# Kernel tuning notes

Measured on AMD Instinct MI355X. Metric: run time of the kernel, lower is better.

Reference implementation:

```python
import jax, jax.numpy as jnp
import numpy as np

B, FEW, D = 128, 64, 512
E, O, H, K = 16, 512, 64, 3


def setup_inputs() -> dict:
    key = jax.random.key(0)
    ks = jax.random.split(key, 9)
    s_d = 1.0 / np.sqrt(D)
    s_h = 1.0 / np.sqrt(H)
    x = jax.random.normal(ks[0], (B, FEW, D), dtype=jnp.float32)
    # gating network params (Linear(D,64), Linear(64,E))
    gW1 = jax.random.uniform(ks[1], (D, H), jnp.float32, -s_d, s_d)
    gb1 = jax.random.uniform(ks[2], (H,), jnp.float32, -s_d, s_d)
    gW2 = jax.random.uniform(ks[3], (H, E), jnp.float32, -s_h, s_h)
    gb2 = jax.random.uniform(ks[4], (E,), jnp.float32, -s_h, s_h)
    # stacked expert params: fc1 Linear(D,64), fc2 Linear(64,O) per expert
    W1 = jax.random.uniform(ks[5], (E, D, H), jnp.float32, -s_d, s_d)
    b1 = jax.random.uniform(ks[6], (E, H), jnp.float32, -s_d, s_d)
    W2 = jax.random.uniform(ks[7], (E, H, O), jnp.float32, -s_h, s_h)
    b2 = jax.random.uniform(ks[8], (E, O), jnp.float32, -s_h, s_h)
    return {"x": x, "gW1": gW1, "gb1": gb1, "gW2": gW2, "gb2": gb2,
            "W1": W1, "b1": b1, "W2": W2, "b2": b2}


def reference(x, gW1, gb1, gW2, gb2, W1, b1, W2, b2):
    b, few, d = x.shape
    t = x.reshape(b * few, d)                                   # [T, D]
    # gating: relu(Linear) -> Linear -> softmax over experts
    gates = jax.nn.softmax(jax.nn.relu(t @ gW1 + gb1) @ gW2 + gb2, axis=-1)
    gates = gates.reshape(b, few, -1)                           # [B, few, E]
    # dense all-expert compute (matches torch stack over ModuleList)
    h = jax.nn.relu(jnp.einsum('td,edh->teh', t, W1) + b1)      # [T, E, H]
    eo = jnp.einsum('teh,eho->teo', h, W2) + b2                 # [T, E, O]
    eo = eo.reshape(b, few, eo.shape[1], -1)                    # [B, few, E, O]
    # top-k gate values and gather corresponding expert outputs
    topv, topi = jax.lax.top_k(gates, K)                        # [B, few, K]
    sel = jnp.take_along_axis(eo, topi[..., None], axis=2)      # [B, few, K, O]
    out = jnp.sum(sel * topv[..., None], axis=2)                # [B, few, O]
    out = jnp.mean(out, axis=1, keepdims=True)                  # [B, 1, O]
    return out[:, :, None, :]                                   # [B, 1, 1, O]
```

## Files before the change

kernel.cpp:

```cpp
#include <hip/hip_runtime.h>
#include <math.h>

constexpr int Bn  = 128;
constexpr int FEW = 64;
constexpr int Dd  = 512;
constexpr int En  = 16;
constexpr int On  = 512;
constexpr int Hn  = 64;
constexpr int Tn  = Bn * FEW;


__global__ __launch_bounds__(256) void k_gate(
    const float* __restrict__ x, const float* __restrict__ gW1,
    const float* __restrict__ gb1, const float* __restrict__ gW2,
    const float* __restrict__ gb2, int* __restrict__ topi,
    float* __restrict__ topv)
{
    __shared__ float g1l[16 * 65];
    __shared__ float logl[16 * 17];
    __shared__ float w2l[64 * 16];
    __shared__ float b2l[16];

    const int tid = threadIdx.x;
    const int ln  = tid & 63;
    const int wv  = tid >> 6;
    const int t0  = blockIdx.x * 16;
    const int tw  = __builtin_amdgcn_readfirstlane(t0 + wv * 4);

    #pragma unroll
    for (int k = 0; k < 4; k++) w2l[tid + k * 256] = gW2[tid + k * 256];
    if (tid < 16) b2l[tid] = gb2[tid];

    float acc[4];
    const float gb1v = gb1[ln];
    #pragma unroll
    for (int i = 0; i < 4; i++) acc[i] = gb1v;

    const float* xt0 = x + (size_t)tw * Dd;

    float  wc[8];
    float4 xa[4], xb[4];
    #pragma unroll
    for (int j = 0; j < 8; j++) wc[j] = gW1[j * 64 + ln];
    #pragma unroll
    for (int i = 0; i < 4; i++) {
        xa[i] = *(const float4*)(xt0 + i * Dd);
        xb[i] = *(const float4*)(xt0 + i * Dd + 4);
    }

    for (int d = 0; d < 512; d += 8) {
        const int dn = (d + 8) & 511;
        float  wn[8];
        float4 xc[4], xd[4];
        #pragma unroll
        for (int j = 0; j < 8; j++) wn[j] = gW1[(dn + j) * 64 + ln];
        #pragma unroll
        for (int i = 0; i < 4; i++) {
            xc[i] = *(const float4*)(xt0 + i * Dd + dn);
            xd[i] = *(const float4*)(xt0 + i * Dd + dn + 4);
        }
        #pragma unroll
        for (int j = 0; j < 4; j++)
            #pragma unroll
            for (int i = 0; i < 4; i++)
                acc[i] = fmaf(((const float*)&xa[i])[j], wc[j], acc[i]);
        #pragma unroll
        for (int j = 0; j < 4; j++)
            #pragma unroll
            for (int i = 0; i < 4; i++)
                acc[i] = fmaf(((const float*)&xb[i])[j], wc[j + 4], acc[i]);
        #pragma unroll
        for (int j = 0; j < 8; j++) wc[j] = wn[j];
        #pragma unroll
        for (int i = 0; i < 4; i++) { xa[i] = xc[i]; xb[i] = xd[i]; }
    }

    #pragma unroll
    for (int i = 0; i < 4; i++) g1l[(wv * 4 + i) * 65 + ln] = fmaxf(acc[i], 0.f);
    __syncthreads();

    {
        const int tok = tid >> 4;
        const int e   = tid & 15;
        float s = b2l[e];
        const float* g = &g1l[tok * 65];
        #pragma unroll 8
        for (int h = 0; h < 64; h++) s = fmaf(g[h], w2l[h * 16 + e], s);
        logl[tok * 17 + e] = s;
    }
    __syncthreads();

    if (tid < 16) {
        float v[16];
        float mx = -1e30f;
        #pragma unroll
        for (int e = 0; e < 16; e++) { v[e] = logl[tid * 17 + e]; mx = fmaxf(mx, v[e]); }
        float ssum = 0.f;
        #pragma unroll
        for (int e = 0; e < 16; e++) { v[e] = __expf(v[e] - mx); ssum += v[e]; }
        const float inv = 1.f / ssum;
        #pragma unroll
        for (int e = 0; e < 16; e++) v[e] *= inv;
        const int t = t0 + tid;
        unsigned mask = 0;
        for (int j = 0; j < 3; j++) {
            float bv = -1.f; int bi = 0;
            for (int e = 0; e < 16; e++) {
                if (!(mask & (1u << e)) && v[e] > bv) { bv = v[e]; bi = e; }
            }
            mask |= (1u << bi);
            topi[t * 4 + j] = bi;
            topv[t * 4 + j] = bv;
        }
    }
}

__global__ __launch_bounds__(256) void k_expert(
    const float* __restrict__ x, const float* __restrict__ W1,
    const float* __restrict__ b1, const int* __restrict__ topi,
    const float* __restrict__ topv, float* __restrict__ A,
    float* __restrict__ gsum)
{
    __shared__ int   lt[128];
    __shared__ float lv[128];
    __shared__ float Ap[2 * 64];
    __shared__ float gp[2];
    __shared__ int   cnt;

    const int tid = threadIdx.x;
    const int ln  = tid & 63;
    const int wv  = tid >> 6;
    const int e   = blockIdx.x >> 6;
    const int s   = blockIdx.x & 63;
    const int ts  = s * 128;

    if (tid == 0) cnt = 0;
    if (tid < 128) Ap[tid] = 0.f;
    if (tid < 2) gp[tid] = 0.f;
    __syncthreads();

    if (tid < 128) {
        const int t = ts + tid;
        const int4   ti = *(const int4*)(topi + t * 4);
        const float4 tv = *(const float4*)(topv + t * 4);
        const int   idx[3] = { ti.x, ti.y, ti.z };
        const float val[3] = { tv.x, tv.y, tv.z };
        #pragma unroll
        for (int j = 0; j < 3; j++) {
            if (idx[j] == e) {
                const int p = atomicAdd(&cnt, 1);
                lt[p] = tid;
                lv[p] = val[j];
                atomicAdd(&gp[tid >> 6], val[j]);
            }
        }
    }
    __syncthreads();
    const int n = cnt;

    const float b1v = b1[e * 64 + ln];
    const float* __restrict__ W1e = W1 + (size_t)e * (Dd * Hn);

    for (int r0 = wv * 8; r0 < n; r0 += 32) {
        const float* xt[8];
        float mvv[8];
        int   bl[8];
        #pragma unroll
        for (int i = 0; i < 8; i++) {
            const int p = r0 + i;
            int   t = (p < n) ? lt[p] : 0;
            float v = (p < n) ? lv[p] : 0.f;
            t = __builtin_amdgcn_readfirstlane(t);
            xt[i]  = x + (size_t)(ts + t) * Dd;
            mvv[i] = v;
            bl[i]  = t >> 6;
        }
        float acc[8];
        #pragma unroll
        for (int i = 0; i < 8; i++) acc[i] = 0.f;

        float  wc[4];
        float4 xc[8];
        #pragma unroll
        for (int j = 0; j < 4; j++) wc[j] = W1e[j * 64 + ln];
        #pragma unroll
        for (int i = 0; i < 8; i++) xc[i] = *(const float4*)(xt[i]);

        for (int d = 0; d < 512; d += 4) {
            const int dn = (d + 4) & 511;
            float  wn[4];
            float4 xn[8];
            #pragma unroll
            for (int j = 0; j < 4; j++) wn[j] = W1e[(dn + j) * 64 + ln];
            #pragma unroll
            for (int i = 0; i < 8; i++) xn[i] = *(const float4*)(xt[i] + dn);
            #pragma unroll
            for (int j = 0; j < 4; j++)
                #pragma unroll
                for (int i = 0; i < 8; i++)
                    acc[i] = fmaf(((const float*)&xc[i])[j], wc[j], acc[i]);
            #pragma unroll
            for (int j = 0; j < 4; j++) wc[j] = wn[j];
            #pragma unroll
            for (int i = 0; i < 8; i++) xc[i] = xn[i];
        }

        #pragma unroll
        for (int i = 0; i < 8; i++) {
            const float h = fmaxf(acc[i] + b1v, 0.f);
            atomicAdd(&Ap[bl[i] * 64 + ln], mvv[i] * h);
        }
    }
    __syncthreads();

    if (tid < 128) {
        const int bl2 = tid >> 6, h = tid & 63;
        A[(size_t)(s * 2 + bl2) * (En * Hn) + e * 64 + h] = Ap[tid];
    }
    if (tid < 2) gsum[(s * 2 + tid) * En + e] = gp[tid];
}

__global__ __launch_bounds__(256) void k_out(
    const float* __restrict__ W2, const float* __restrict__ b2,
    const float* __restrict__ A, const float* __restrict__ gsum,
    float* __restrict__ out)
{
    __shared__ float Al[4096];
    __shared__ float gl[64];

    const int tid = threadIdx.x;
    const int bq  = blockIdx.x >> 3;
    const int oc  = blockIdx.x & 7;
    const int b0  = bq * 4;
    const int bh  = tid >> 6;
    const int o   = oc * 64 + (tid & 63);

    #pragma unroll
    for (int k = 0; k < 4; k++)
        ((float4*)Al)[tid + k * 256] = ((const float4*)(A + (size_t)b0 * 1024))[tid + k * 256];
    if (tid < 64) gl[tid] = gsum[b0 * En + tid];
    __syncthreads();

    const int ab = bh * 1024;
    float a = 0.f;
    const float* w2p = W2 + o;

    float wc[8];
    #pragma unroll
    for (int j = 0; j < 8; j++) wc[j] = w2p[j * On];

    for (int eh = 0; eh < 1024; eh += 8) {
        const int en = (eh + 8) & 1023;
        float wn[8];
        #pragma unroll
        for (int j = 0; j < 8; j++) wn[j] = w2p[(size_t)(en + j) * On];
        #pragma unroll
        for (int j = 0; j < 8; j++) a = fmaf(Al[ab + eh + j], wc[j], a);
        #pragma unroll
        for (int j = 0; j < 8; j++) wc[j] = wn[j];
    }
    #pragma unroll
    for (int ee = 0; ee < 16; ee++) a = fmaf(gl[bh * 16 + ee], b2[ee * On + o], a);

    out[(size_t)(b0 + bh) * On + o] = a * (1.f / 64.f);
}

extern "C" void kernel_launch(void* const* d_in, const int* in_sizes, int n_in,
                              void* d_out, int out_size, void* d_ws, size_t ws_size,
                              hipStream_t stream)
{
    (void)in_sizes; (void)n_in; (void)out_size; (void)ws_size;
    const float* x   = (const float*)d_in[0];
    const float* gW1 = (const float*)d_in[1];
    const float* gb1 = (const float*)d_in[2];
    const float* gW2 = (const float*)d_in[3];
    const float* gb2 = (const float*)d_in[4];
    const float* W1  = (const float*)d_in[5];
    const float* b1  = (const float*)d_in[6];
    const float* W2  = (const float*)d_in[7];
    const float* b2  = (const float*)d_in[8];
    float* out = (float*)d_out;

    char* ws = (char*)d_ws;
    int*   topi = (int*)(ws);
    float* topv = (float*)(ws + 131072);
    float* A    = (float*)(ws + 262144);
    float* gsum = (float*)(ws + 786432);

    k_gate  <<<dim3(512),  dim3(256), 0, stream>>>(x, gW1, gb1, gW2, gb2, topi, topv);
    k_expert<<<dim3(1024), dim3(256), 0, stream>>>(x, W1, b1, topi, topv, A, gsum);
    k_out   <<<dim3(256),  dim3(256), 0, stream>>>(W2, b2, A, gsum, out);
}
```

Before: 245.5 us.

## Stage token activations and expert weights in LDS for gate and expert kernels

The gate kernel now loads its 16 tokens' activations into shared memory and reads them from LDS, where before each wave read them straight from global memory. The expert kernel tiles W1 into 128-row LDS chunks shared by all four waves, and stages the gathered token rows into LDS, so each weight element is fetched from global memory once per block rather than once per wave. The output kernel switches to vectorized float4 LDS reads. The cost is extra __syncthreads barriers and a much larger LDS footprint (about 48KB in the expert kernel), which can lower occupancy, and there is no double buffering to hide the load latency.

```diff
diff --git a/kernel.cpp b/kernel.cpp
--- a/kernel.cpp
+++ b/kernel.cpp
@@ -1,13 +1,10 @@
 #include <hip/hip_runtime.h>
 #include <math.h>
 
-constexpr int Bn  = 128;
-constexpr int FEW = 64;
 constexpr int Dd  = 512;
 constexpr int En  = 16;
 constexpr int On  = 512;
 constexpr int Hn  = 64;
-constexpr int Tn  = Bn * FEW;
 
 
 __global__ __launch_bounds__(256) void k_gate(
@@ -16,6 +13,7 @@
     const float* __restrict__ gb2, int* __restrict__ topi,
     float* __restrict__ topv)
 {
+    __shared__ float xlds[16 * 512];
     __shared__ float g1l[16 * 65];
     __shared__ float logl[16 * 17];
     __shared__ float w2l[64 * 16];
@@ -25,54 +23,45 @@
     const int ln  = tid & 63;
     const int wv  = tid >> 6;
     const int t0  = blockIdx.x * 16;
-    const int tw  = __builtin_amdgcn_readfirstlane(t0 + wv * 4);
 
     #pragma unroll
     for (int k = 0; k < 4; k++) w2l[tid + k * 256] = gW2[tid + k * 256];
     if (tid < 16) b2l[tid] = gb2[tid];
 
+    #pragma unroll
+    for (int k = 0; k < 8; k++) {
+        const int f   = tid + k * 256;
+        const int tok = f >> 7;
+        const int df4 = f & 127;
+        ((float4*)xlds)[f] =
+            *(const float4*)(x + (size_t)(t0 + tok) * Dd + df4 * 4);
+    }
+    __syncthreads();
+
     float acc[4];
     const float gb1v = gb1[ln];
     #pragma unroll
     for (int i = 0; i < 4; i++) acc[i] = gb1v;
 
-    const float* xt0 = x + (size_t)tw * Dd;
-
-    float  wc[8];
-    float4 xa[4], xb[4];
-    #pragma unroll
-    for (int j = 0; j < 8; j++) wc[j] = gW1[j * 64 + ln];
-    #pragma unroll
-    for (int i = 0; i < 4; i++) {
-        xa[i] = *(const float4*)(xt0 + i * Dd);
-        xb[i] = *(const float4*)(xt0 + i * Dd + 4);
-    }
-
-    for (int d = 0; d < 512; d += 8) {
-        const int dn = (d + 8) & 511;
-        float  wn[8];
-        float4 xc[4], xd[4];
-        #pragma unroll
-        for (int j = 0; j < 8; j++) wn[j] = gW1[(dn + j) * 64 + ln];
+    float w[4];
+    #pragma unroll
+    for (int j = 0; j < 4; j++) w[j] = gW1[j * 64 + ln];
+
+    for (int dq = 0; dq < 512; dq += 4) {
+        const int dn = (dq + 4) & 511;
+        float wn[4];
+        #pragma unroll
+        for (int j = 0; j < 4; j++) wn[j] = gW1[(dn + j) * 64 + ln];
         #pragma unroll
         for (int i = 0; i < 4; i++) {
-            xc[i] = *(const float4*)(xt0 + i * Dd + dn);
-            xd[i] = *(const float4*)(xt0 + i * Dd + dn + 4);
-        }
-        #pragma unroll
-        for (int j = 0; j < 4; j++)
-            #pragma unroll
-            for (int i = 0; i < 4; i++)
-                acc[i] = fmaf(((const float*)&xa[i])[j], wc[j], acc[i]);
-        #pragma unroll
-        for (int j = 0; j < 4; j++)
-            #pragma unroll
-            for (int i = 0; i < 4; i++)
-                acc[i] = fmaf(((const float*)&xb[i])[j], wc[j + 4], acc[i]);
-        #pragma unroll
-        for (int j = 0; j < 8; j++) wc[j] = wn[j];
-        #pragma unroll
-        for (int i = 0; i < 4; i++) { xa[i] = xc[i]; xb[i] = xd[i]; }
+            const float4 xv = *(const float4*)&xlds[(wv * 4 + i) * 512 + dq];
+            acc[i] = fmaf(xv.x, w[0], acc[i]);
+            acc[i] = fmaf(xv.y, w[1], acc[i]);
+            acc[i] = fmaf(xv.z, w[2], acc[i]);
+            acc[i] = fmaf(xv.w, w[3], acc[i]);
+        }
+        #pragma unroll
+        for (int j = 0; j < 4; j++) w[j] = wn[j];
     }
 
     #pragma unroll
@@ -121,6 +110,8 @@
     const float* __restrict__ topv, float* __restrict__ A,
     float* __restrict__ gsum)
 {
+    __shared__ float wlds[128 * 64];
+    __shared__ float xlds[32 * 128];
     __shared__ int   lt[128];
     __shared__ float lv[128];
     __shared__ float Ap[2 * 64];
@@ -161,54 +152,56 @@
     const float b1v = b1[e * 64 + ln];
     const float* __restrict__ W1e = W1 + (size_t)e * (Dd * Hn);
 
-    for (int r0 = wv * 8; r0 < n; r0 += 32) {
-        const float* xt[8];
-        float mvv[8];
-        int   bl[8];
+    for (int bs = 0; bs < n; bs += 32) {
+        int   tt[8]; float mv[8]; int bl[8];
         #pragma unroll
         for (int i = 0; i < 8; i++) {
-            const int p = r0 + i;
-            int   t = (p < n) ? lt[p] : 0;
-            float v = (p < n) ? lv[p] : 0.f;
-            t = __builtin_amdgcn_readfirstlane(t);
-            xt[i]  = x + (size_t)(ts + t) * Dd;
-            mvv[i] = v;
-            bl[i]  = t >> 6;
+            const int slot = bs + wv * 8 + i;
+            tt[i] = (slot < n) ? lt[slot] : 0;
+            mv[i] = (slot < n) ? lv[slot] : 0.f;
+            bl[i] = tt[i] >> 6;
         }
         float acc[8];
         #pragma unroll
         for (int i = 0; i < 8; i++) acc[i] = 0.f;
 
-        float  wc[4];
-        float4 xc[8];
-        #pragma unroll
-        for (int j = 0; j < 4; j++) wc[j] = W1e[j * 64 + ln];
-        #pragma unroll
-        for (int i = 0; i < 8; i++) xc[i] = *(const float4*)(xt[i]);
-
-        for (int d = 0; d < 512; d += 4) {
-            const int dn = (d + 4) & 511;
-            float  wn[4];
-            float4 xn[8];
+        for (int c = 0; c < 4; c++) {
+            __syncthreads();
             #pragma unroll
-            for (int j = 0; j < 4; j++) wn[j] = W1e[(dn + j) * 64 + ln];
+            for (int k = 0; k < 8; k++)
+                ((float4*)wlds)[tid + k * 256] =
+                    ((const float4*)(W1e + c * 8192))[tid + k * 256];
             #pragma unroll
-            for (int i = 0; i < 8; i++) xn[i] = *(const float4*)(xt[i] + dn);
-            #pragma unroll
-            for (int j = 0; j < 4; j++)
+            for (int k = 0; k < 4; k++) {
+                const int f    = tid + k * 256;
+                const int tokl = f >> 5;
+                const int df4  = f & 31;
+                const int tg   = (bs + tokl < n) ? lt[bs + tokl] : 0;
+                ((float4*)xlds)[f] =
+                    *(const float4*)(x + (size_t)(ts + tg) * Dd + c * 128 + df4 * 4);
+            }
+            __syncthreads();
+
+            for (int dq = 0; dq < 128; dq += 4) {
+                const float w0 = wlds[(dq + 0) * 64 + ln];
+                const float w1 = wlds[(dq + 1) * 64 + ln];
+                const float w2 = wlds[(dq + 2) * 64 + ln];
+                const float w3 = wlds[(dq + 3) * 64 + ln];
                 #pragma unroll
-                for (int i = 0; i < 8; i++)
-                    acc[i] = fmaf(((const float*)&xc[i])[j], wc[j], acc[i]);
-            #pragma unroll
-            for (int j = 0; j < 4; j++) wc[j] = wn[j];
-            #pragma unroll
-            for (int i = 0; i < 8; i++) xc[i] = xn[i];
+                for (int i = 0; i < 8; i++) {
+                    const float4 xv = *(const float4*)&xlds[(wv * 8 + i) * 128 + dq];
+                    acc[i] = fmaf(xv.x, w0, acc[i]);
+                    acc[i] = fmaf(xv.y, w1, acc[i]);
+                    acc[i] = fmaf(xv.z, w2, acc[i]);
+                    acc[i] = fmaf(xv.w, w3, acc[i]);
+                }
+            }
         }
 
         #pragma unroll
         for (int i = 0; i < 8; i++) {
             const float h = fmaxf(acc[i] + b1v, 0.f);
-            atomicAdd(&Ap[bl[i] * 64 + ln], mvv[i] * h);
+            atomicAdd(&Ap[bl[i] * 64 + ln], mv[i] * h);
         }
     }
     __syncthreads();
@@ -229,11 +222,12 @@
     __shared__ float gl[64];
 
     const int tid = threadIdx.x;
+    const int ln  = tid & 63;
+    const int wv  = tid >> 6;
     const int bq  = blockIdx.x >> 3;
     const int oc  = blockIdx.x & 7;
     const int b0  = bq * 4;
-    const int bh  = tid >> 6;
-    const int o   = oc * 64 + (tid & 63);
+    const int o   = oc * 64 + ln;
 
     #pragma unroll
     for (int k = 0; k < 4; k++)
@@ -241,28 +235,36 @@
     if (tid < 64) gl[tid] = gsum[b0 * En + tid];
     __syncthreads();
 
-    const int ab = bh * 1024;
+    const int ab = wv * 1024;
+    const float* w2p = W2 + o;
     float a = 0.f;
-    const float* w2p = W2 + o;
 
     float wc[8];
     #pragma unroll
-    for (int j = 0; j < 8; j++) wc[j] = w2p[j * On];
+    for (int j = 0; j < 8; j++) wc[j] = w2p[(size_t)j * On];
 
     for (int eh = 0; eh < 1024; eh += 8) {
         const int en = (eh + 8) & 1023;
         float wn[8];
         #pragma unroll
         for (int j = 0; j < 8; j++) wn[j] = w2p[(size_t)(en + j) * On];
-        #pragma unroll
-        for (int j = 0; j < 8; j++) a = fmaf(Al[ab + eh + j], wc[j], a);
+        const float4 a0 = *(const float4*)&Al[ab + eh];
+        const float4 a1 = *(const float4*)&Al[ab + eh + 4];
+        a = fmaf(a0.x, wc[0], a);
+        a = fmaf(a0.y, wc[1], a);
+        a = fmaf(a0.z, wc[2], a);
+        a = fmaf(a0.w, wc[3], a);
+        a = fmaf(a1.x, wc[4], a);
+        a = fmaf(a1.y, wc[5], a);
+        a = fmaf(a1.z, wc[6], a);
+        a = fmaf(a1.w, wc[7], a);
         #pragma unroll
         for (int j = 0; j < 8; j++) wc[j] = wn[j];
     }
     #pragma unroll
-    for (int ee = 0; ee < 16; ee++) a = fmaf(gl[bh * 16 + ee], b2[ee * On + o], a);
-
-    out[(size_t)(b0 + bh) * On + o] = a * (1.f / 64.f);
+    for (int ee = 0; ee < 16; ee++) a = fmaf(gl[wv * 16 + ee], b2[ee * On + o], a);
+
+    out[(size_t)(b0 + wv) * On + o] = a * (1.f / 64.f);
 }
 
 extern "C" void kernel_launch(void* const* d_in, const int* in_sizes, int n_in,
```

Measured after the change: 259.3 us. 1.06x slower.

## Use 4x4 register tiles for gate and expert GEMMs, drop LDS staging in output

Applied to the files above, without the earlier changes.

The gate and expert kernels now give each thread a 4-token by 4-hidden register tile with float4 weight loads, in place of one hidden unit per lane across several tokens. Each block handles more tokens (64 in the gate, 256 per expert slice), so fewer blocks are launched. The aim is to raise FMA-to-load intensity and reuse each weight load across tokens. The output kernel reads A and gsum straight from global memory with float4 prefetch instead of staging them in shared memory. The risks are lower occupancy and parallelism from fewer blocks, higher register pressure, and uncoalesced per-thread x row loads.

```diff
diff --git a/kernel.cpp b/kernel.cpp
--- a/kernel.cpp
+++ b/kernel.cpp
@@ -1,13 +1,10 @@
 #include <hip/hip_runtime.h>
 #include <math.h>
 
-constexpr int Bn  = 128;
-constexpr int FEW = 64;
 constexpr int Dd  = 512;
 constexpr int En  = 16;
 constexpr int On  = 512;
 constexpr int Hn  = 64;
-constexpr int Tn  = Bn * FEW;
 
 
 __global__ __launch_bounds__(256) void k_gate(
@@ -16,81 +13,102 @@
     const float* __restrict__ gb2, int* __restrict__ topi,
     float* __restrict__ topv)
 {
-    __shared__ float g1l[16 * 65];
-    __shared__ float logl[16 * 17];
+    __shared__ float g1l[64 * 68];
+    __shared__ float logl[64 * 17];
     __shared__ float w2l[64 * 16];
     __shared__ float b2l[16];
 
     const int tid = threadIdx.x;
-    const int ln  = tid & 63;
-    const int wv  = tid >> 6;
-    const int t0  = blockIdx.x * 16;
-    const int tw  = __builtin_amdgcn_readfirstlane(t0 + wv * 4);
+    const int st  = tid & 15;
+    const int th  = tid >> 4;
+    const int t0  = blockIdx.x * 64;
+    const int tb  = t0 + st * 4;
 
     #pragma unroll
     for (int k = 0; k < 4; k++) w2l[tid + k * 256] = gW2[tid + k * 256];
     if (tid < 16) b2l[tid] = gb2[tid];
 
-    float acc[4];
-    const float gb1v = gb1[ln];
-    #pragma unroll
-    for (int i = 0; i < 4; i++) acc[i] = gb1v;
-
-    const float* xt0 = x + (size_t)tw * Dd;
-
-    float  wc[8];
-    float4 xa[4], xb[4];
-    #pragma unroll
-    for (int j = 0; j < 8; j++) wc[j] = gW1[j * 64 + ln];
+    float acc[4][4];
+    #pragma unroll
+    for (int c = 0; c < 4; c++) {
+        const float bv = gb1[th * 4 + c];
+        #pragma unroll
+        for (int i = 0; i < 4; i++) acc[i][c] = bv;
+    }
+
+    const float* xb[4];
+    #pragma unroll
+    for (int i = 0; i < 4; i++) xb[i] = x + (size_t)(tb + i) * Dd;
+    const float* wb = gW1 + th * 4;
+
+    float4 xcA[4], xcB[4], wc[8];
+    #pragma unroll
+    for (int j = 0; j < 8; j++) wc[j] = *(const float4*)(wb + j * 64);
     #pragma unroll
     for (int i = 0; i < 4; i++) {
-        xa[i] = *(const float4*)(xt0 + i * Dd);
-        xb[i] = *(const float4*)(xt0 + i * Dd + 4);
+        xcA[i] = *(const float4*)(xb[i]);
+        xcB[i] = *(const float4*)(xb[i] + 4);
     }
 
     for (int d = 0; d < 512; d += 8) {
         const int dn = (d + 8) & 511;
-        float  wn[8];
-        float4 xc[4], xd[4];
-        #pragma unroll
-        for (int j = 0; j < 8; j++) wn[j] = gW1[(dn + j) * 64 + ln];
+        float4 xnA[4], xnB[4], wn[8];
+        #pragma unroll
+        for (int j = 0; j < 8; j++) wn[j] = *(const float4*)(wb + (dn + j) * 64);
         #pragma unroll
         for (int i = 0; i < 4; i++) {
-            xc[i] = *(const float4*)(xt0 + i * Dd + dn);
-            xd[i] = *(const float4*)(xt0 + i * Dd + dn + 4);
+            xnA[i] = *(const float4*)(xb[i] + dn);
+            xnB[i] = *(const float4*)(xb[i] + dn + 4);
         }
         #pragma unroll
         for (int j = 0; j < 4; j++)
             #pragma unroll
-            for (int i = 0; i < 4; i++)
-                acc[i] = fmaf(((const float*)&xa[i])[j], wc[j], acc[i]);
+            for (int i = 0; i < 4; i++) {
+                const float xv = ((const float*)&xcA[i])[j];
+                #pragma unroll
+                for (int c = 0; c < 4; c++)
+                    acc[i][c] = fmaf(xv, ((const float*)&wc[j])[c], acc[i][c]);
+            }
         #pragma unroll
         for (int j = 0; j < 4; j++)
             #pragma unroll
-            for (int i = 0; i < 4; i++)
-                acc[i] = fmaf(((const float*)&xb[i])[j], wc[j + 4], acc[i]);
+            for (int i = 0; i < 4; i++) {
+                const float xv = ((const float*)&xcB[i])[j];
+                #pragma unroll
+                for (int c = 0; c < 4; c++)
+                    acc[i][c] = fmaf(xv, ((const float*)&wc[j + 4])[c], acc[i][c]);
+            }
         #pragma unroll
         for (int j = 0; j < 8; j++) wc[j] = wn[j];
         #pragma unroll
-        for (int i = 0; i < 4; i++) { xa[i] = xc[i]; xb[i] = xd[i]; }
-    }
-
-    #pragma unroll
-    for (int i = 0; i < 4; i++) g1l[(wv * 4 + i) * 65 + ln] = fmaxf(acc[i], 0.f);
-    __syncthreads();
-
-    {
-        const int tok = tid >> 4;
-        const int e   = tid & 15;
-        float s = b2l[e];
-        const float* g = &g1l[tok * 65];
+        for (int i = 0; i < 4; i++) { xcA[i] = xnA[i]; xcB[i] = xnB[i]; }
+    }
+
+    #pragma unroll
+    for (int i = 0; i < 4; i++) {
+        float4 hv;
+        hv.x = fmaxf(acc[i][0], 0.f);
+        hv.y = fmaxf(acc[i][1], 0.f);
+        hv.z = fmaxf(acc[i][2], 0.f);
+        hv.w = fmaxf(acc[i][3], 0.f);
+        *(float4*)&g1l[(st * 4 + i) * 68 + th * 4] = hv;
+    }
+    __syncthreads();
+
+    #pragma unroll
+    for (int q = 0; q < 4; q++) {
+        const int lid = tid + q * 256;
+        const int tok = lid >> 4;
+        const int e   = lid & 15;
+        float sacc = b2l[e];
+        const float* g = &g1l[tok * 68];
         #pragma unroll 8
-        for (int h = 0; h < 64; h++) s = fmaf(g[h], w2l[h * 16 + e], s);
-        logl[tok * 17 + e] = s;
-    }
-    __syncthreads();
-
-    if (tid < 16) {
+        for (int h = 0; h < 64; h++) sacc = fmaf(g[h], w2l[h * 16 + e], sacc);
+        logl[tok * 17 + e] = sacc;
+    }
+    __syncthreads();
+
+    if (tid < 64) {
         float v[16];
         float mx = -1e30f;
         #pragma unroll
@@ -121,25 +139,25 @@
     const float* __restrict__ topv, float* __restrict__ A,
     float* __restrict__ gsum)
 {
-    __shared__ int   lt[128];
-    __shared__ float lv[128];
-    __shared__ float Ap[2 * 64];
-    __shared__ float gp[2];
+    __shared__ int   lt[256];
+    __shared__ float lv[256];
+    __shared__ float Ap[4 * 64];
+    __shared__ float gp[4];
     __shared__ int   cnt;
 
     const int tid = threadIdx.x;
-    const int ln  = tid & 63;
-    const int wv  = tid >> 6;
-    const int e   = blockIdx.x >> 6;
-    const int s   = blockIdx.x & 63;
-    const int ts  = s * 128;
+    const int st  = tid & 15;
+    const int th  = tid >> 4;
+    const int e   = blockIdx.x >> 5;
+    const int s   = blockIdx.x & 31;
+    const int ts  = s * 256;
 
     if (tid == 0) cnt = 0;
-    if (tid < 128) Ap[tid] = 0.f;
-    if (tid < 2) gp[tid] = 0.f;
-    __syncthreads();
-
-    if (tid < 128) {
+    Ap[tid] = 0.f;
+    if (tid < 4) gp[tid] = 0.f;
+    __syncthreads();
+
+    {
         const int t = ts + tid;
         const int4   ti = *(const int4*)(topi + t * 4);
         const float4 tv = *(const float4*)(topv + t * 4);
@@ -158,66 +176,71 @@
     __syncthreads();
     const int n = cnt;
 
-    const float b1v = b1[e * 64 + ln];
+    float b1f[4];
+    #pragma unroll
+    for (int c = 0; c < 4; c++) b1f[c] = b1[e * 64 + th * 4 + c];
     const float* __restrict__ W1e = W1 + (size_t)e * (Dd * Hn);
-
-    for (int r0 = wv * 8; r0 < n; r0 += 32) {
-        const float* xt[8];
-        float mvv[8];
-        int   bl[8];
-        #pragma unroll
-        for (int i = 0; i < 8; i++) {
-            const int p = r0 + i;
-            int   t = (p < n) ? lt[p] : 0;
-            float v = (p < n) ? lv[p] : 0.f;
-            t = __builtin_amdgcn_readfirstlane(t);
-            xt[i]  = x + (size_t)(ts + t) * Dd;
-            mvv[i] = v;
-            bl[i]  = t >> 6;
-        }
-        float acc[8];
-        #pragma unroll
-        for (int i = 0; i < 8; i++) acc[i] = 0.f;
-
-        float  wc[4];
-        float4 xc[8];
-        #pragma unroll
-        for (int j = 0; j < 4; j++) wc[j] = W1e[j * 64 + ln];
-        #pragma unroll
-        for (int i = 0; i < 8; i++) xc[i] = *(const float4*)(xt[i]);
+    const float* wb = W1e + th * 4;
+
+    for (int bs = 0; bs < n; bs += 64) {
+        float gv[4]; int bl[4]; const float* xb[4];
+        #pragma unroll
+        for (int i = 0; i < 4; i++) {
+            const int sl = bs + st * 4 + i;
+            const int tt = (sl < n) ? lt[sl] : 0;
+            gv[i] = (sl < n) ? lv[sl] : 0.f;
+            bl[i] = tt >> 6;
+            xb[i] = x + (size_t)(ts + tt) * Dd;
+        }
+        float acc[4][4];
+        #pragma unroll
+        for (int i = 0; i < 4; i++)
+            #pragma unroll
+            for (int c = 0; c < 4; c++) acc[i][c] = 0.f;
+
+        float4 xc[4], wc[4];
+        #pragma unroll
+        for (int j = 0; j < 4; j++) wc[j] = *(const float4*)(wb + j * 64);
+        #pragma unroll
+        for (int i = 0; i < 4; i++) xc[i] = *(const float4*)(xb[i]);
 
         for (int d = 0; d < 512; d += 4) {
             const int dn = (d + 4) & 511;
-            float  wn[4];
-            float4 xn[8];
-            #pragma unroll
-            for (int j = 0; j < 4; j++) wn[j] = W1e[(dn + j) * 64 + ln];
-            #pragma unroll
-            for (int i = 0; i < 8; i++) xn[i] = *(const float4*)(xt[i] + dn);
+            float4 xn[4], wn[4];
+            #pragma unroll
+            for (int j = 0; j < 4; j++) wn[j] = *(const float4*)(wb + (dn + j) * 64);
+            #pragma unroll
+            for (int i = 0; i < 4; i++) xn[i] = *(const float4*)(xb[i] + dn);
             #pragma unroll
             for (int j = 0; j < 4; j++)
                 #pragma unroll
-                for (int i = 0; i < 8; i++)
-                    acc[i] = fmaf(((const float*)&xc[i])[j], wc[j], acc[i]);
+                for (int i = 0; i < 4; i++) {
+                    const float xv = ((const float*)&xc[i])[j];
+                    #pragma unroll
+                    for (int c = 0; c < 4; c++)
+                        acc[i][c] = fmaf(xv, ((const float*)&wc[j])[c], acc[i][c]);
+                }
             #pragma unroll
             for (int j = 0; j < 4; j++) wc[j] = wn[j];
             #pragma unroll
-            for (int i = 0; i < 8; i++) xc[i] = xn[i];
-        }
-
-        #pragma unroll
-        for (int i = 0; i < 8; i++) {
-            const float h = fmaxf(acc[i] + b1v, 0.f);
-            atomicAdd(&Ap[bl[i] * 64 + ln], mvv[i] * h);
-        }
-    }
-    __syncthreads();
-
-    if (tid < 128) {
+            for (int i = 0; i < 4; i++) xc[i] = xn[i];
+        }
+
+        #pragma unroll
+        for (int i = 0; i < 4; i++)
+            #pragma unroll
+            for (int c = 0; c < 4; c++) {
+                const float h = fmaxf(acc[i][c] + b1f[c], 0.f);
+                atomicAdd(&Ap[bl[i] * 64 + th * 4 + c], gv[i] * h);
+            }
+    }
+    __syncthreads();
+
+    {
         const int bl2 = tid >> 6, h = tid & 63;
-        A[(size_t)(s * 2 + bl2) * (En * Hn) + e * 64 + h] = Ap[tid];
-    }
-    if (tid < 2) gsum[(s * 2 + tid) * En + e] = gp[tid];
+        A[(size_t)(s * 4 + bl2) * (En * Hn) + e * 64 + h] = Ap[tid];
+    }
+    if (tid < 4) gsum[(s * 4 + tid) * En + e] = gp[tid];
 }
 
 __global__ __launch_bounds__(256) void k_out(
@@ -225,44 +248,48 @@
     const float* __restrict__ A, const float* __restrict__ gsum,
     float* __restrict__ out)
 {
-    __shared__ float Al[4096];
-    __shared__ float gl[64];
-
     const int tid = threadIdx.x;
+    const int ln  = tid & 63;
+    const int wv  = tid >> 6;
     const int bq  = blockIdx.x >> 3;
     const int oc  = blockIdx.x & 7;
-    const int b0  = bq * 4;
-    const int bh  = tid >> 6;
-    const int o   = oc * 64 + (tid & 63);
-
-    #pragma unroll
-    for (int k = 0; k < 4; k++)
-        ((float4*)Al)[tid + k * 256] = ((const float4*)(A + (size_t)b0 * 1024))[tid + k * 256];
-    if (tid < 64) gl[tid] = gsum[b0 * En + tid];
-    __syncthreads();
-
-    const int ab = bh * 1024;
+    const int b   = bq * 4 + wv;
+    const int o   = oc * 64 + ln;
+
+    const float* Ab  = A + (size_t)b * 1024;
+    const float* w2p = W2 + o;
     float a = 0.f;
-    const float* w2p = W2 + o;
-
-    float wc[8];
-    #pragma unroll
-    for (int j = 0; j < 8; j++) wc[j] = w2p[j * On];
+
+    float wcv[8];
+    float4 a0 = *(const float4*)(Ab);
+    float4 a1 = *(const float4*)(Ab + 4);
+    #pragma unroll
+    for (int j = 0; j < 8; j++) wcv[j] = w2p[(size_t)j * On];
 
     for (int eh = 0; eh < 1024; eh += 8) {
         const int en = (eh + 8) & 1023;
         float wn[8];
+        float4 a0n = *(const float4*)(Ab + en);
+        float4 a1n = *(const float4*)(Ab + en + 4);
         #pragma unroll
         for (int j = 0; j < 8; j++) wn[j] = w2p[(size_t)(en + j) * On];
-        #pragma unroll
-        for (int j = 0; j < 8; j++) a = fmaf(Al[ab + eh + j], wc[j], a);
-        #pragma unroll
-        for (int j = 0; j < 8; j++) wc[j] = wn[j];
-    }
-    #pragma unroll
-    for (int ee = 0; ee < 16; ee++) a = fmaf(gl[bh * 16 + ee], b2[ee * On + o], a);
-
-    out[(size_t)(b0 + bh) * On + o] = a * (1.f / 64.f);
+        a = fmaf(a0.x, wcv[0], a);
+        a = fmaf(a0.y, wcv[1], a);
+        a = fmaf(a0.z, wcv[2], a);
+        a = fmaf(a0.w, wcv[3], a);
+        a = fmaf(a1.x, wcv[4], a);
+        a = fmaf(a1.y, wcv[5], a);
+        a = fmaf(a1.z, wcv[6], a);
+        a = fmaf(a1.w, wcv[7], a);
+        #pragma unroll
+        for (int j = 0; j < 8; j++) wcv[j] = wn[j];
+        a0 = a0n; a1 = a1n;
+    }
+    const float* gb = gsum + (size_t)b * En;
+    #pragma unroll
+    for (int ee = 0; ee < 16; ee++) a = fmaf(gb[ee], b2[ee * On + o], a);
+
+    out[(size_t)b * On + o] = a * (1.f / 64.f);
 }
 
 extern "C" void kernel_launch(void* const* d_in, const int* in_sizes, int n_in,
@@ -287,7 +314,7 @@
     float* A    = (float*)(ws + 262144);
     float* gsum = (float*)(ws + 786432);
 
-    k_gate  <<<dim3(512),  dim3(256), 0, stream>>>(x, gW1, gb1, gW2, gb2, topi, topv);
-    k_expert<<<dim3(1024), dim3(256), 0, stream>>>(x, W1, b1, topi, topv, A, gsum);
-    k_out   <<<dim3(256),  dim3(256), 0, stream>>>(W2, b2, A, gsum, out);
+    k_gate  <<<dim3(128), dim3(256), 0, stream>>>(x, gW1, gb1, gW2, gb2, topi, topv);
+    k_expert<<<dim3(512), dim3(256), 0, stream>>>(x, W1, b1, topi, topv, A, gsum);
+    k_out   <<<dim3(256), dim3(256), 0, stream>>>(W2, b2, A, gsum, out);
 }
```

Result: slower. 452.3 us (+84.2%).
